# Kernel optimization log

Hardware: AMD Instinct MI355X
Metric: run time of the kernel (lower is better)

The kernel has to match this reference:

```python
import jax, jax.numpy as jnp
import numpy as np

S, B, L, D, H, NOP = 4, 8, 512, 128, 128, 64  # segments, batch, seg_len, input_dim, hidden, n_operators
W = S * L  # 2048 total words
FT = 0.1   # forget-gate floor


def _norm_mat(m):
    # divide each row by its count of nonzero entries (torch normalize_matrix)
    cnt = (m != 0).sum(-1, keepdims=True).astype(m.dtype)
    return m / (cnt + 1e-30)


def _l2(x):
    return x / (jnp.linalg.norm(x, axis=-1, keepdims=True) + 1e-30)


def setup_inputs() -> dict:
    key = jax.random.key(0)
    ks = jax.random.split(key, 16)
    word_outputs = jax.random.normal(ks[0], (S, B, L, D), jnp.float32)
    node_hidden = jax.random.normal(ks[1], (B, D), jnp.float32)
    op_embedding = jax.random.normal(ks[2], (B, NOP, D), jnp.float32)
    word_operator = (jax.random.uniform(ks[3], (B, W, NOP)) < 0.05).astype(jnp.float32)
    word_word = (jax.random.uniform(ks[4], (B, W, W)) < 0.02).astype(jnp.float32)
    depend_relation = (jax.random.uniform(ks[5], (S, B, L, L)) < 0.05).astype(jnp.float32)
    word_exist_matrix = (jax.random.uniform(ks[6], (B, W, W)) < 0.9).astype(jnp.float32)
    word_exist_sequence = (jax.random.uniform(ks[7], (B, W)) < 0.9).astype(jnp.float32)
    goal_word = (jax.random.uniform(ks[8], (B, W)) < 0.2).astype(jnp.float32)

    def lin(k, fi, fo):
        k1, k2 = jax.random.split(k)
        s = 1.0 / np.sqrt(fi).astype(np.float32)
        return (jax.random.uniform(k1, (fi, fo), jnp.float32, -s, s),
                jax.random.uniform(k2, (fo,), jnp.float32, -s, s))

    o_w_W, o_w_b = lin(ks[9], D, H)
    wk_W, wk_b = lin(ks[10], D, H)
    ws_W, ws_b = lin(ks[11], D, H)
    up_W, up_b = lin(ks[12], 3 * H, D)
    wg_W, wg_b = lin(ks[13], D, D)
    fg_W, fg_b = lin(ks[14], 2 * D, D)
    return dict(word_outputs=word_outputs, node_hidden=node_hidden, op_embedding=op_embedding,
                word_operator=word_operator, word_word=word_word, depend_relation=depend_relation,
                word_exist_matrix=word_exist_matrix, word_exist_sequence=word_exist_sequence,
                goal_word=goal_word, o_w_W=o_w_W, o_w_b=o_w_b, wk_W=wk_W, wk_b=wk_b,
                ws_W=ws_W, ws_b=ws_b, up_W=up_W, up_b=up_b, wg_W=wg_W, wg_b=wg_b,
                fg_W=fg_W, fg_b=fg_b)


def reference(word_outputs, node_hidden, op_embedding, word_operator, word_word,
              depend_relation, word_exist_matrix, word_exist_sequence, goal_word,
              o_w_W, o_w_b, wk_W, wk_b, ws_W, ws_b, up_W, up_b, wg_W, wg_b, fg_W, fg_b):
    # cat(word_outputs, dim=1) -> [B, W, D]
    all_word = word_outputs.transpose(1, 0, 2, 3).reshape(B, W, D)
    # operator aggregation: [B,W,NOP] @ o_w(op_embedding) -> [B,W,H], L2-normalized
    word_o = _l2(jnp.einsum('bwo,boh->bwh', word_operator, op_embedding @ o_w_W + o_w_b))
    # knowledge aggregation over masked word-word adjacency
    adj_k = _norm_mat(word_word * word_exist_matrix)
    word_w_k = _l2(jnp.einsum('bvw,bwh->bvh', adj_k, all_word @ wk_W + wk_b))
    # per-segment dependency aggregation, then concat along word dim
    seg = jnp.einsum('sbij,sbjh->sbih', _norm_mat(depend_relation), word_outputs @ ws_W + ws_b)
    word_w_s = _l2(seg.transpose(1, 0, 2, 3).reshape(B, W, H))
    neighbor = jnp.concatenate([word_o, word_w_k, word_w_s], axis=-1)  # [B, W, 3H]
    word_updated = jax.nn.relu(neighbor @ up_W + up_b)  # [B, W, D]
    # goal pooling: bmm([B,1,W],[B,W,D]) -> [B,D]
    gw = _norm_mat(goal_word * word_exist_sequence)
    goal_w = jnp.einsum('bw,bwd->bd', gw, word_updated)
    goal_updated = jax.nn.relu(goal_w @ wg_W + wg_b)
    forget = jax.nn.sigmoid(jnp.concatenate([goal_w, node_hidden], axis=-1) @ fg_W + fg_b)
    return jnp.maximum(forget, FT) * node_hidden + (1.0 - forget) * goal_updated
```

## Files before the change

### kernel.cpp

```cpp
#include <hip/hip_runtime.h>
#include <math.h>

#define Sn 4
#define Bn 8
#define Ln 512
#define Dn 128
#define Hn 128
#define NOPn 64
#define Wn 2048


__device__ __forceinline__ float bf2f(unsigned short u) {
    return __uint_as_float(((unsigned int)u) << 16);
}
__device__ __forceinline__ unsigned short f2bf(float f) {
    unsigned int u = __float_as_uint(f);
    return (unsigned short)((u + 0x7FFFu + ((u >> 16) & 1u)) >> 16);
}

__global__ __launch_bounds__(256) void prep_k(const float* __restrict__ A,
                                              const float* __restrict__ W1,
                                              const float* __restrict__ W2,
                                              const float* __restrict__ b1,
                                              const float* __restrict__ b2,
                                              unsigned short* __restrict__ C1,
                                              unsigned short* __restrict__ C2,
                                              const float* __restrict__ ope,
                                              const float* __restrict__ owW,
                                              const float* __restrict__ owb,
                                              unsigned short* __restrict__ oph,
                                              const float* __restrict__ goal,
                                              const float* __restrict__ wes,
                                              int* __restrict__ widx,
                                              int* __restrict__ wcnt,
                                              float* __restrict__ gwacc,
                                              const float* __restrict__ upW,
                                              unsigned short* __restrict__ upWbf) {
    __shared__ __align__(16) float lA[32][68];
    __shared__ __align__(16) float lW1[32][132];
    __shared__ __align__(16) float lW2[32][132];
    __shared__ int cnt;
    const int bid = blockIdx.x, tid = threadIdx.x;

    if (bid < 256) {
        const int m0 = bid * 64;
        float acc1[4][8] = {}, acc2[4][8] = {};
        const int r0 = (tid & 15) * 4;
        const int h0 = (tid >> 4) * 8;
        for (int k0 = 0; k0 < 128; k0 += 32) {
            __syncthreads();
            {
                const int r = tid >> 2, kk = (tid & 3) * 8;
                const float* src = A + (size_t)(m0 + r) * 128 + (k0 + kk);
                float4 v0 = reinterpret_cast<const float4*>(src)[0];
                float4 v1 = reinterpret_cast<const float4*>(src)[1];
                lA[kk + 0][r] = v0.x; lA[kk + 1][r] = v0.y;
                lA[kk + 2][r] = v0.z; lA[kk + 3][r] = v0.w;
                lA[kk + 4][r] = v1.x; lA[kk + 5][r] = v1.y;
                lA[kk + 6][r] = v1.z; lA[kk + 7][r] = v1.w;
            }
            {
                const int kk = tid >> 3, hh = (tid & 7) * 16;
                const float* s1 = W1 + (size_t)(k0 + kk) * 128 + hh;
                const float* s2 = W2 + (size_t)(k0 + kk) * 128 + hh;
#pragma unroll
                for (int q = 0; q < 4; ++q) {
                    float4 v1 = reinterpret_cast<const float4*>(s1)[q];
                    float4 v2 = reinterpret_cast<const float4*>(s2)[q];
                    lW1[kk][hh + 4 * q + 0] = v1.x; lW1[kk][hh + 4 * q + 1] = v1.y;
                    lW1[kk][hh + 4 * q + 2] = v1.z; lW1[kk][hh + 4 * q + 3] = v1.w;
                    lW2[kk][hh + 4 * q + 0] = v2.x; lW2[kk][hh + 4 * q + 1] = v2.y;
                    lW2[kk][hh + 4 * q + 2] = v2.z; lW2[kk][hh + 4 * q + 3] = v2.w;
                }
            }
            __syncthreads();
#pragma unroll
            for (int k = 0; k < 32; ++k) {
                float4 a   = *reinterpret_cast<const float4*>(&lA[k][r0]);
                float4 w10 = *reinterpret_cast<const float4*>(&lW1[k][h0]);
                float4 w11 = *reinterpret_cast<const float4*>(&lW1[k][h0 + 4]);
                float4 w20 = *reinterpret_cast<const float4*>(&lW2[k][h0]);
                float4 w21 = *reinterpret_cast<const float4*>(&lW2[k][h0 + 4]);
                float av[4] = {a.x, a.y, a.z, a.w};
                float wv1[8] = {w10.x, w10.y, w10.z, w10.w, w11.x, w11.y, w11.z, w11.w};
                float wv2[8] = {w20.x, w20.y, w20.z, w20.w, w21.x, w21.y, w21.z, w21.w};
#pragma unroll
                for (int i = 0; i < 4; ++i)
#pragma unroll
                    for (int j = 0; j < 8; ++j) {
                        acc1[i][j] = fmaf(av[i], wv1[j], acc1[i][j]);
                        acc2[i][j] = fmaf(av[i], wv2[j], acc2[i][j]);
                    }
            }
        }
#pragma unroll
        for (int i = 0; i < 4; ++i) {
            alignas(16) unsigned short u1[8], u2[8];
#pragma unroll
            for (int j = 0; j < 8; ++j) {
                u1[j] = f2bf(acc1[i][j] + b1[h0 + j]);
                u2[j] = f2bf(acc2[i][j] + b2[h0 + j]);
            }
            const size_t off = (size_t)(m0 + r0 + i) * 128 + h0;
            *reinterpret_cast<uint4*>(C1 + off) = *reinterpret_cast<const uint4*>(u1);
            *reinterpret_cast<uint4*>(C2 + off) = *reinterpret_cast<const uint4*>(u2);
        }
    } else if (bid < 264) {
        const int m0 = (bid - 256) * 64;
        float acc[4][8] = {};
        const int r0 = (tid & 15) * 4;
        const int h0 = (tid >> 4) * 8;
        for (int k0 = 0; k0 < 128; k0 += 32) {
            __syncthreads();
            {
                const int r = tid >> 2, kk = (tid & 3) * 8;
                const float* src = ope + (size_t)(m0 + r) * 128 + (k0 + kk);
                float4 v0 = reinterpret_cast<const float4*>(src)[0];
                float4 v1 = reinterpret_cast<const float4*>(src)[1];
                lA[kk + 0][r] = v0.x; lA[kk + 1][r] = v0.y;
                lA[kk + 2][r] = v0.z; lA[kk + 3][r] = v0.w;
                lA[kk + 4][r] = v1.x; lA[kk + 5][r] = v1.y;
                lA[kk + 6][r] = v1.z; lA[kk + 7][r] = v1.w;
            }
            {
                const int kk = tid >> 3, hh = (tid & 7) * 16;
                const float* src = owW + (size_t)(k0 + kk) * 128 + hh;
#pragma unroll
                for (int q = 0; q < 4; ++q) {
                    float4 v = reinterpret_cast<const float4*>(src)[q];
                    lW1[kk][hh + 4 * q + 0] = v.x; lW1[kk][hh + 4 * q + 1] = v.y;
                    lW1[kk][hh + 4 * q + 2] = v.z; lW1[kk][hh + 4 * q + 3] = v.w;
                }
            }
            __syncthreads();
#pragma unroll
            for (int k = 0; k < 32; ++k) {
                float4 a  = *reinterpret_cast<const float4*>(&lA[k][r0]);
                float4 w0 = *reinterpret_cast<const float4*>(&lW1[k][h0]);
                float4 w1 = *reinterpret_cast<const float4*>(&lW1[k][h0 + 4]);
                float av[4] = {a.x, a.y, a.z, a.w};
                float wv[8] = {w0.x, w0.y, w0.z, w0.w, w1.x, w1.y, w1.z, w1.w};
#pragma unroll
                for (int i = 0; i < 4; ++i)
#pragma unroll
                    for (int j = 0; j < 8; ++j) acc[i][j] = fmaf(av[i], wv[j], acc[i][j]);
            }
        }
#pragma unroll
        for (int i = 0; i < 4; ++i) {
            alignas(16) unsigned short us[8];
#pragma unroll
            for (int j = 0; j < 8; ++j) us[j] = f2bf(acc[i][j] + owb[h0 + j]);
            *reinterpret_cast<uint4*>(oph + (size_t)(m0 + r0 + i) * 128 + h0) =
                *reinterpret_cast<const uint4*>(us);
        }
    } else if (bid < 272) {
        const int b = bid - 264;
        if (tid == 0) cnt = 0;
        __syncthreads();
#pragma unroll
        for (int j = 0; j < 8; ++j) {
            const int w = tid * 8 + j;
            if (goal[b * Wn + w] != 0.f && wes[b * Wn + w] != 0.f) {
                const int p = atomicAdd(&cnt, 1);
                if (p < 512) widx[b * 512 + p] = w;
            }
        }
        __syncthreads();
        if (tid == 0) wcnt[b] = cnt < 512 ? cnt : 512;
    } else if (bid == 272) {
        for (int idx = tid; idx < 1024; idx += 256) gwacc[idx] = 0.f;
    } else {
        const int base = (bid - 273) * 24576;
        for (int e = base + tid * 4; e < base + 24576; e += 1024) {
            float4 v = *reinterpret_cast<const float4*>(upW + e);
            alignas(8) unsigned short u[4] = {f2bf(v.x), f2bf(v.y), f2bf(v.z), f2bf(v.w)};
            *reinterpret_cast<uint2*>(upWbf + e) = *reinterpret_cast<const uint2*>(u);
        }
    }
}

__global__ __launch_bounds__(256) void mega_agg4(const int* __restrict__ widx,
                                                 const int* __restrict__ wcnt,
                                                 const float* __restrict__ ww,
                                                 const float* __restrict__ wem,
                                                 const float* __restrict__ dep,
                                                 const float* __restrict__ wop,
                                                 const unsigned short* __restrict__ oph,
                                                 const unsigned short* __restrict__ wkh,
                                                 const unsigned short* __restrict__ wsh,
                                                 const unsigned short* __restrict__ upWbf,
                                                 const float* __restrict__ upb,
                                                 float* __restrict__ gwacc) {
    const int slot = blockIdx.x;
    const int b = slot >> 9, i = slot & 511;
    if (i >= wcnt[b]) return;
    const int w_dst = widx[slot];
    const int t = threadIdx.x;
    const int lane = t & 63, wv = t >> 6;

    __shared__ int kidx[512];
    __shared__ int sidx[256];
    __shared__ int kn, sn;
    __shared__ float part1[4][128];
    __shared__ float part2[4][128];
    __shared__ float nbL[384];
    __shared__ float gpart[4][128];
    if (t == 0) { kn = 0; sn = 0; }
    __syncthreads();

    const float* wwr = ww  + ((size_t)(b * Wn + w_dst)) * Wn;
    const float* wmr = wem + ((size_t)(b * Wn + w_dst)) * Wn;
#pragma unroll
    for (int q = 0; q < 2; ++q) {
        const int e0 = q * 1024 + t * 4;
        float4 v = *reinterpret_cast<const float4*>(wwr + e0);
        float4 m = *reinterpret_cast<const float4*>(wmr + e0);
        float vv[4] = {v.x, v.y, v.z, v.w};
        float mm[4] = {m.x, m.y, m.z, m.w};
#pragma unroll
        for (int j = 0; j < 4; ++j)
            if (vv[j] != 0.f && mm[j] != 0.f) {
                int p = atomicAdd(&kn, 1);
                if (p < 512) kidx[p] = e0 + j;
            }
    }
    const int sD = w_dst >> 9, lD = w_dst & 511;
    if (t < 128) {
        const float* dr = dep + ((size_t)((sD * Bn + b) * Ln + lD)) * Ln + t * 4;
        float4 v = *reinterpret_cast<const float4*>(dr);
        float vv[4] = {v.x, v.y, v.z, v.w};
#pragma unroll
        for (int j = 0; j < 4; ++j)
            if (vv[j] != 0.f) {
                int p = atomicAdd(&sn, 1);
                if (p < 256) sidx[p] = t * 4 + j;
            }
    }
    float m_op = 0.f;
    if (wv == 3) m_op = wop[((size_t)(b * Wn + w_dst)) * NOPn + lane];
    __syncthreads();

    const int nk = kn < 512 ? kn : 512;
    const int ns = sn < 256 ? sn : 256;

    {
        float a0 = 0.f, a1 = 0.f;
        for (int p = wv; p < nk; p += 4) {
            const int w = kidx[p];
            const int s = w >> 9, l = w & 511;
            ushort2 x = *reinterpret_cast<const ushort2*>(
                wkh + ((size_t)((s * Bn + b) * Ln + l)) * Hn + 2 * lane);
            a0 += bf2f(x.x);
            a1 += bf2f(x.y);
        }
        part1[wv][2 * lane]     = a0;
        part1[wv][2 * lane + 1] = a1;
    }
    {
        const unsigned short* base = wsh + (size_t)((sD * Bn + b) * Ln) * Hn + 2 * lane;
        float a0 = 0.f, a1 = 0.f;
        for (int p = wv; p < ns; p += 4) {
            ushort2 x = *reinterpret_cast<const ushort2*>(base + (size_t)sidx[p] * Hn);
            a0 += bf2f(x.x);
            a1 += bf2f(x.y);
        }
        part2[wv][2 * lane]     = a0;
        part2[wv][2 * lane + 1] = a1;
    }
    if (wv == 3) {
        unsigned long long bal = __ballot(m_op != 0.f);
        float a0 = 0.f, a1 = 0.f;
        const unsigned short* base = oph + (size_t)b * NOPn * Hn + 2 * lane;
        while (bal) {
            const int o = __ffsll(bal) - 1;
            bal &= bal - 1;
            ushort2 v = *reinterpret_cast<const ushort2*>(base + o * Hn);
            a0 += bf2f(v.x);
            a1 += bf2f(v.y);
        }
        float ss = a0 * a0 + a1 * a1;
#pragma unroll
        for (int off = 1; off < 64; off <<= 1) ss += __shfl_xor(ss, off);
        const float sc = 1.f / (sqrtf(ss) + 1e-30f);
        nbL[2 * lane]     = a0 * sc;
        nbL[2 * lane + 1] = a1 * sc;
    }
    __syncthreads();

    if (wv == 0) {
        float s0 = 0.f, s1 = 0.f;
#pragma unroll
        for (int q = 0; q < 4; ++q) {
            s0 += part1[q][2 * lane];
            s1 += part1[q][2 * lane + 1];
        }
        float ss = s0 * s0 + s1 * s1;
#pragma unroll
        for (int off = 1; off < 64; off <<= 1) ss += __shfl_xor(ss, off);
        const float sc = 1.f / (sqrtf(ss) + 1e-30f);
        nbL[128 + 2 * lane]     = s0 * sc;
        nbL[128 + 2 * lane + 1] = s1 * sc;
    } else if (wv == 1) {
        float s0 = 0.f, s1 = 0.f;
#pragma unroll
        for (int q = 0; q < 4; ++q) {
            s0 += part2[q][2 * lane];
            s1 += part2[q][2 * lane + 1];
        }
        float ss = s0 * s0 + s1 * s1;
#pragma unroll
        for (int off = 1; off < 64; off <<= 1) ss += __shfl_xor(ss, off);
        const float sc = 1.f / (sqrtf(ss) + 1e-30f);
        nbL[256 + 2 * lane]     = s0 * sc;
        nbL[256 + 2 * lane + 1] = s1 * sc;
    }
    __syncthreads();

    {
        const int q = t >> 6, d0 = t & 63;
        float a0 = 0.f, a1 = 0.f;
        const unsigned short* wp = upWbf + (size_t)(q * 96) * 128;
#pragma unroll 8
        for (int k = 0; k < 96; ++k) {
            const float x = nbL[q * 96 + k];
            a0 = fmaf(x, bf2f(wp[(size_t)k * 128 + d0]), a0);
            a1 = fmaf(x, bf2f(wp[(size_t)k * 128 + 64 + d0]), a1);
        }
        gpart[q][d0]      = a0;
        gpart[q][64 + d0] = a1;
    }
    __syncthreads();
    if (t < 128) {
        const float g = fmaxf(gpart[0][t] + gpart[1][t] + gpart[2][t] + gpart[3][t]
                              + upb[t], 0.f);
        atomicAdd(&gwacc[b * 128 + t], g);
    }
}

__global__ __launch_bounds__(128) void final4_k(const int* __restrict__ wcnt,
                                                const float* __restrict__ gwacc,
                                                const float* __restrict__ nh,
                                                const float* __restrict__ wgW,
                                                const float* __restrict__ wgb,
                                                const float* __restrict__ fgW,
                                                const float* __restrict__ fgb,
                                                float* __restrict__ out) {
    const int b = blockIdx.x, t = threadIdx.x;
    __shared__ float gw[Dn], nhs[Dn];
    const float inv = 1.f / ((float)wcnt[b] + 1e-30f);
    gw[t]  = gwacc[b * Dn + t] * inv;
    nhs[t] = nh[b * Dn + t];
    __syncthreads();
    float gu = wgb[t];
    for (int d = 0; d < Dn; ++d) gu = fmaf(gw[d], wgW[d * Dn + t], gu);
    gu = fmaxf(gu, 0.f);
    float fg = fgb[t];
    for (int d = 0; d < Dn; ++d) fg = fmaf(gw[d], fgW[d * Dn + t], fg);
    for (int d = 0; d < Dn; ++d) fg = fmaf(nhs[d], fgW[(Dn + d) * Dn + t], fg);
    const float forget = 1.f / (1.f + expf(-fg));
    out[b * Dn + t] = fmaxf(forget, 0.1f) * nhs[t] + (1.f - forget) * gu;
}

extern "C" void kernel_launch(void* const* d_in, const int* in_sizes, int n_in,
                              void* d_out, int out_size, void* d_ws, size_t ws_size,
                              hipStream_t stream) {
    (void)in_sizes; (void)n_in; (void)out_size; (void)ws_size;
    const float* word_outputs        = (const float*)d_in[0];
    const float* node_hidden         = (const float*)d_in[1];
    const float* op_embedding        = (const float*)d_in[2];
    const float* word_operator       = (const float*)d_in[3];
    const float* word_word           = (const float*)d_in[4];
    const float* depend_relation     = (const float*)d_in[5];
    const float* word_exist_matrix   = (const float*)d_in[6];
    const float* word_exist_sequence = (const float*)d_in[7];
    const float* goal_word           = (const float*)d_in[8];
    const float* o_w_W = (const float*)d_in[9];
    const float* o_w_b = (const float*)d_in[10];
    const float* wk_W  = (const float*)d_in[11];
    const float* wk_b  = (const float*)d_in[12];
    const float* ws_W  = (const float*)d_in[13];
    const float* ws_b  = (const float*)d_in[14];
    const float* up_W  = (const float*)d_in[15];
    const float* up_b  = (const float*)d_in[16];
    const float* wg_W  = (const float*)d_in[17];
    const float* wg_b  = (const float*)d_in[18];
    const float* fg_W  = (const float*)d_in[19];
    const float* fg_b  = (const float*)d_in[20];
    float* out = (float*)d_out;

    char* ws = (char*)d_ws;
    unsigned short* oph   = (unsigned short*)(ws + 0);
    unsigned short* wkh   = (unsigned short*)(ws + (1u << 20));
    unsigned short* wsh   = (unsigned short*)(ws + (5u << 20));
    int* widx             = (int*)(ws + (9u << 20));
    int* wcnt             = (int*)(ws + (9u << 20) + 32768);
    float* gwacc          = (float*)(ws + (9u << 20) + 65536);
    unsigned short* upWbf = (unsigned short*)(ws + (9u << 20) + 131072);

    prep_k<<<275, 256, 0, stream>>>(word_outputs, wk_W, ws_W, wk_b, ws_b, wkh, wsh,
                                    op_embedding, o_w_W, o_w_b, oph,
                                    goal_word, word_exist_sequence, widx, wcnt, gwacc,
                                    up_W, upWbf);
    mega_agg4<<<4096, 256, 0, stream>>>(widx, wcnt, word_word, word_exist_matrix,
                                        depend_relation, word_operator, oph, wkh, wsh,
                                        upWbf, up_b, gwacc);
    final4_k<<<8, 128, 0, stream>>>(wcnt, gwacc, node_hidden,
                                    wg_W, wg_b, fg_W, fg_b, out);
}
```

Measured before the change: 350.6 us.

## Process one destination word per wavefront instead of per block

Restructures the aggregation kernel so each 64-lane wavefront handles one goal word end to end, packing four words per block and cutting the grid from 4096 to 1024 blocks. This removes all block-level __syncthreads and the cross-wave partial-sum reductions through shared memory. The up-projection matvec is rewritten to read 8 bf16 weights per lane with uint4 loads and reduce with shuffles. In exchange, each wave walks its full neighbor lists serially, which may expose more memory latency per word. Per-wave shared state is initialized and read without any barrier, relying on wavefront lockstep execution.

```diff
diff --git a/kernel.cpp b/kernel.cpp
--- a/kernel.cpp
+++ b/kernel.cpp
@@ -12,6 +12,12 @@
 
 __device__ __forceinline__ float bf2f(unsigned short u) {
     return __uint_as_float(((unsigned int)u) << 16);
+}
+__device__ __forceinline__ float bflo(unsigned int u) {
+    return __uint_as_float(u << 16);
+}
+__device__ __forceinline__ float bfhi(unsigned int u) {
+    return __uint_as_float(u & 0xFFFF0000u);
 }
 __device__ __forceinline__ unsigned short f2bf(float f) {
     unsigned int u = __float_as_uint(f);
@@ -180,7 +186,7 @@
     }
 }
 
-__global__ __launch_bounds__(256) void mega_agg4(const int* __restrict__ widx,
+__global__ __launch_bounds__(256) void mega_agg8(const int* __restrict__ widx,
                                                  const int* __restrict__ wcnt,
                                                  const float* __restrict__ ww,
                                                  const float* __restrict__ wem,
@@ -192,28 +198,27 @@
                                                  const unsigned short* __restrict__ upWbf,
                                                  const float* __restrict__ upb,
                                                  float* __restrict__ gwacc) {
-    const int slot = blockIdx.x;
-    const int b = slot >> 9, i = slot & 511;
+    const int bid = blockIdx.x;
+    const int b = bid & 7;
+    const int t = threadIdx.x;
+    const int lane = t & 63, w = t >> 6;
+    const int i = (bid >> 3) * 4 + w;
+
+    __shared__ int kidxL[4][512];
+    __shared__ int sidxL[4][256];
+    __shared__ float nbLL[4][384];
+    __shared__ int knL[4], snL[4];
+
     if (i >= wcnt[b]) return;
-    const int w_dst = widx[slot];
-    const int t = threadIdx.x;
-    const int lane = t & 63, wv = t >> 6;
-
-    __shared__ int kidx[512];
-    __shared__ int sidx[256];
-    __shared__ int kn, sn;
-    __shared__ float part1[4][128];
-    __shared__ float part2[4][128];
-    __shared__ float nbL[384];
-    __shared__ float gpart[4][128];
-    if (t == 0) { kn = 0; sn = 0; }
-    __syncthreads();
+    const int w_dst = widx[b * 512 + i];
+
+    if (lane == 0) { knL[w] = 0; snL[w] = 0; }
 
     const float* wwr = ww  + ((size_t)(b * Wn + w_dst)) * Wn;
     const float* wmr = wem + ((size_t)(b * Wn + w_dst)) * Wn;
 #pragma unroll
-    for (int q = 0; q < 2; ++q) {
-        const int e0 = q * 1024 + t * 4;
+    for (int q = 0; q < 8; ++q) {
+        const int e0 = q * 256 + lane * 4;
         float4 v = *reinterpret_cast<const float4*>(wwr + e0);
         float4 m = *reinterpret_cast<const float4*>(wmr + e0);
         float vv[4] = {v.x, v.y, v.z, v.w};
@@ -221,54 +226,27 @@
 #pragma unroll
         for (int j = 0; j < 4; ++j)
             if (vv[j] != 0.f && mm[j] != 0.f) {
-                int p = atomicAdd(&kn, 1);
-                if (p < 512) kidx[p] = e0 + j;
+                const int p = atomicAdd(&knL[w], 1);
+                if (p < 512) kidxL[w][p] = e0 + j;
             }
     }
     const int sD = w_dst >> 9, lD = w_dst & 511;
-    if (t < 128) {
-        const float* dr = dep + ((size_t)((sD * Bn + b) * Ln + lD)) * Ln + t * 4;
-        float4 v = *reinterpret_cast<const float4*>(dr);
+    const float* dr = dep + ((size_t)((sD * Bn + b) * Ln + lD)) * Ln;
+#pragma unroll
+    for (int q = 0; q < 2; ++q) {
+        const int e0 = q * 256 + lane * 4;
+        float4 v = *reinterpret_cast<const float4*>(dr + e0);
         float vv[4] = {v.x, v.y, v.z, v.w};
 #pragma unroll
         for (int j = 0; j < 4; ++j)
             if (vv[j] != 0.f) {
-                int p = atomicAdd(&sn, 1);
-                if (p < 256) sidx[p] = t * 4 + j;
-            }
-    }
-    float m_op = 0.f;
-    if (wv == 3) m_op = wop[((size_t)(b * Wn + w_dst)) * NOPn + lane];
-    __syncthreads();
-
-    const int nk = kn < 512 ? kn : 512;
-    const int ns = sn < 256 ? sn : 256;
+                const int p = atomicAdd(&snL[w], 1);
+                if (p < 256) sidxL[w][p] = e0 + j;
+            }
+    }
 
     {
-        float a0 = 0.f, a1 = 0.f;
-        for (int p = wv; p < nk; p += 4) {
-            const int w = kidx[p];
-            const int s = w >> 9, l = w & 511;
-            ushort2 x = *reinterpret_cast<const ushort2*>(
-                wkh + ((size_t)((s * Bn + b) * Ln + l)) * Hn + 2 * lane);
-            a0 += bf2f(x.x);
-            a1 += bf2f(x.y);
-        }
-        part1[wv][2 * lane]     = a0;
-        part1[wv][2 * lane + 1] = a1;
-    }
-    {
-        const unsigned short* base = wsh + (size_t)((sD * Bn + b) * Ln) * Hn + 2 * lane;
-        float a0 = 0.f, a1 = 0.f;
-        for (int p = wv; p < ns; p += 4) {
-            ushort2 x = *reinterpret_cast<const ushort2*>(base + (size_t)sidx[p] * Hn);
-            a0 += bf2f(x.x);
-            a1 += bf2f(x.y);
-        }
-        part2[wv][2 * lane]     = a0;
-        part2[wv][2 * lane + 1] = a1;
-    }
-    if (wv == 3) {
+        const float m_op = wop[((size_t)(b * Wn + w_dst)) * NOPn + lane];
         unsigned long long bal = __ballot(m_op != 0.f);
         float a0 = 0.f, a1 = 0.f;
         const unsigned short* base = oph + (size_t)b * NOPn * Hn + 2 * lane;
@@ -283,58 +261,73 @@
 #pragma unroll
         for (int off = 1; off < 64; off <<= 1) ss += __shfl_xor(ss, off);
         const float sc = 1.f / (sqrtf(ss) + 1e-30f);
-        nbL[2 * lane]     = a0 * sc;
-        nbL[2 * lane + 1] = a1 * sc;
-    }
-    __syncthreads();
-
-    if (wv == 0) {
-        float s0 = 0.f, s1 = 0.f;
-#pragma unroll
-        for (int q = 0; q < 4; ++q) {
-            s0 += part1[q][2 * lane];
-            s1 += part1[q][2 * lane + 1];
-        }
-        float ss = s0 * s0 + s1 * s1;
+        nbLL[w][2 * lane]     = a0 * sc;
+        nbLL[w][2 * lane + 1] = a1 * sc;
+    }
+
+    const int nk = knL[w] < 512 ? knL[w] : 512;
+    const int ns = snL[w] < 256 ? snL[w] : 256;
+
+    {
+        float a0 = 0.f, a1 = 0.f;
+#pragma unroll 4
+        for (int p = 0; p < nk; ++p) {
+            const int wd = kidxL[w][p];
+            const int s = wd >> 9, l = wd & 511;
+            ushort2 x = *reinterpret_cast<const ushort2*>(
+                wkh + ((size_t)((s * Bn + b) * Ln + l)) * Hn + 2 * lane);
+            a0 += bf2f(x.x);
+            a1 += bf2f(x.y);
+        }
+        float ss = a0 * a0 + a1 * a1;
 #pragma unroll
         for (int off = 1; off < 64; off <<= 1) ss += __shfl_xor(ss, off);
         const float sc = 1.f / (sqrtf(ss) + 1e-30f);
-        nbL[128 + 2 * lane]     = s0 * sc;
-        nbL[128 + 2 * lane + 1] = s1 * sc;
-    } else if (wv == 1) {
-        float s0 = 0.f, s1 = 0.f;
-#pragma unroll
-        for (int q = 0; q < 4; ++q) {
-            s0 += part2[q][2 * lane];
-            s1 += part2[q][2 * lane + 1];
-        }
-        float ss = s0 * s0 + s1 * s1;
+        nbLL[w][128 + 2 * lane]     = a0 * sc;
+        nbLL[w][128 + 2 * lane + 1] = a1 * sc;
+    }
+    {
+        const unsigned short* base = wsh + (size_t)((sD * Bn + b) * Ln) * Hn + 2 * lane;
+        float a0 = 0.f, a1 = 0.f;
+#pragma unroll 4
+        for (int p = 0; p < ns; ++p) {
+            ushort2 x = *reinterpret_cast<const ushort2*>(base + (size_t)sidxL[w][p] * Hn);
+            a0 += bf2f(x.x);
+            a1 += bf2f(x.y);
+        }
+        float ss = a0 * a0 + a1 * a1;
 #pragma unroll
         for (int off = 1; off < 64; off <<= 1) ss += __shfl_xor(ss, off);
         const float sc = 1.f / (sqrtf(ss) + 1e-30f);
-        nbL[256 + 2 * lane]     = s0 * sc;
-        nbL[256 + 2 * lane + 1] = s1 * sc;
-    }
-    __syncthreads();
+        nbLL[w][256 + 2 * lane]     = a0 * sc;
+        nbLL[w][256 + 2 * lane + 1] = a1 * sc;
+    }
 
     {
-        const int q = t >> 6, d0 = t & 63;
-        float a0 = 0.f, a1 = 0.f;
-        const unsigned short* wp = upWbf + (size_t)(q * 96) * 128;
+        const int i8 = (lane & 15) * 8, j = lane >> 4;
+        float a[8] = {};
 #pragma unroll 8
-        for (int k = 0; k < 96; ++k) {
-            const float x = nbL[q * 96 + k];
-            a0 = fmaf(x, bf2f(wp[(size_t)k * 128 + d0]), a0);
-            a1 = fmaf(x, bf2f(wp[(size_t)k * 128 + 64 + d0]), a1);
-        }
-        gpart[q][d0]      = a0;
-        gpart[q][64 + d0] = a1;
-    }
-    __syncthreads();
-    if (t < 128) {
-        const float g = fmaxf(gpart[0][t] + gpart[1][t] + gpart[2][t] + gpart[3][t]
-                              + upb[t], 0.f);
-        atomicAdd(&gwacc[b * 128 + t], g);
+        for (int r = 0; r < 96; ++r) {
+            const int k = r * 4 + j;
+            const uint4 wv4 = *reinterpret_cast<const uint4*>(upWbf + (size_t)k * 128 + i8);
+            const float x = nbLL[w][k];
+            a[0] = fmaf(x, bflo(wv4.x), a[0]); a[1] = fmaf(x, bfhi(wv4.x), a[1]);
+            a[2] = fmaf(x, bflo(wv4.y), a[2]); a[3] = fmaf(x, bfhi(wv4.y), a[3]);
+            a[4] = fmaf(x, bflo(wv4.z), a[4]); a[5] = fmaf(x, bfhi(wv4.z), a[5]);
+            a[6] = fmaf(x, bflo(wv4.w), a[6]); a[7] = fmaf(x, bfhi(wv4.w), a[7]);
+        }
+#pragma unroll
+        for (int q = 0; q < 8; ++q) {
+            a[q] += __shfl_xor(a[q], 16);
+            a[q] += __shfl_xor(a[q], 32);
+        }
+        if (lane < 16) {
+#pragma unroll
+            for (int q = 0; q < 8; ++q) {
+                const float g = fmaxf(a[q] + upb[i8 + q], 0.f);
+                atomicAdd(&gwacc[b * 128 + i8 + q], g);
+            }
+        }
     }
 }
 
@@ -402,7 +395,7 @@
                                     op_embedding, o_w_W, o_w_b, oph,
                                     goal_word, word_exist_sequence, widx, wcnt, gwacc,
                                     up_W, upWbf);
-    mega_agg4<<<4096, 256, 0, stream>>>(widx, wcnt, word_word, word_exist_matrix,
+    mega_agg8<<<1024, 256, 0, stream>>>(widx, wcnt, word_word, word_exist_matrix,
                                         depend_relation, word_operator, oph, wkh, wsh,
                                         upWbf, up_b, gwacc);
     final4_k<<<8, 128, 0, stream>>>(wcnt, gwacc, node_hidden,
```

Measured after the change: 406.4 us. 1.16x slower.
